# Performance work log

Measured on AMD Instinct MI355X. Metric: run time of the kernel, lower is better.

The kernel has to match this reference:

```python
import jax, jax.numpy as jnp
import numpy as np

B, C, N, T = 16, 32, 1024, 64
C_OUT = 32
ORDER = 2
SMOOTH_DEPTH = 1


def setup_inputs() -> dict:
    key = jax.random.key(0)
    k1, k2, k3, k4 = jax.random.split(key, 4)
    x = jax.random.normal(k1, (B, C, N, T), dtype=jnp.float32)
    # row-normalized dense adjacencies (transition matrices), as used in Graph-WaveNet-style supports
    AL = jax.random.uniform(k2, (N, N), dtype=jnp.float32)
    AL = AL / AL.sum(axis=-1, keepdims=True)
    AS_pos = jax.random.uniform(k3, (N, N), dtype=jnp.float32)
    AS_pos = AS_pos / AS_pos.sum(axis=-1, keepdims=True)
    # 1x1 conv mlp: in_channels = (order*support_len+1)*c_in = 3*C, out_channels = C_OUT
    W_mlp = jax.random.normal(k4, (C_OUT, (ORDER + 1) * C), dtype=jnp.float32) * 0.02
    b_mlp = jnp.zeros((C_OUT,), dtype=jnp.float32)
    return {"x": x, "AL": AL, "AS_pos": AS_pos, "W_mlp": W_mlp, "b_mlp": b_mlp}


def reference(x, AL, AS_pos, W_mlp, b_mlp):
    # gcn_module.forward with short_bool=True, smooth_depth=SMOOTH_DEPTH, eval mode (no dropout)
    ALp = jnp.linalg.matrix_power(AL, SMOOTH_DEPTH)          # [N,N]
    # torch.einsum('bckj,ik->bcij', x, ALp): contract node dim of x against ALp
    x_long = jnp.einsum('ik,bckt->bcit', ALp, x)             # [B,C,N,T]
    x_short = x - x_long
    outs = [x]
    for _ in range(ORDER):
        # dnconv: einsum('nvw,ncwl->ncvl', A, x) with 2D A broadcast over batch
        x_long = jnp.einsum('vw,bcwt->bcvt', AL, x_long)
        x_short = jnp.einsum('vw,bcwt->bcvt', AS_pos, x_short)
        outs.append(x_long + x_short)
    h = jnp.concatenate(outs, axis=1)                        # [B,(ORDER+1)*C,N,T]
    # 1x1 conv == channel mixing
    h = jnp.einsum('oc,bcnt->bont', W_mlp, h) + b_mlp[None, :, None, None]
    return h
```

## Files before the change

kernel.cpp:

```cpp
#include <hip/hip_runtime.h>


typedef __bf16 bf16x8 __attribute__((ext_vector_type(8)));
typedef float f32x4 __attribute__((ext_vector_type(4)));
typedef unsigned int u32x4 __attribute__((ext_vector_type(4)));
typedef unsigned int u32x2 __attribute__((ext_vector_type(2)));

__device__ __forceinline__ unsigned short f2bf(float f) {
  unsigned u = __builtin_bit_cast(unsigned, f);
  u += 0x7fffu + ((u >> 16) & 1u);
  return (unsigned short)(u >> 16);
}
__device__ __forceinline__ float bf2f(unsigned short h) {
  unsigned u = ((unsigned)h) << 16;
  return __builtin_bit_cast(float, u);
}

static constexpr size_t OFF_YC    = 0;
static constexpr size_t OFF_ALBF  = 201326592;
static constexpr size_t OFF_ALT   = OFF_ALBF  + 2097152;
static constexpr size_t OFF_ASBF  = OFF_ALT   + 2097152;
static constexpr size_t OFF_AST   = OFF_ASBF  + 2097152;
static constexpr size_t OFF_AL2   = OFF_AST   + 2097152;
static constexpr size_t OFF_AL2T  = OFF_AL2   + 2097152;
static constexpr size_t OFF_ASAL  = OFF_AL2T  + 2097152;
static constexpr size_t OFF_AS2   = OFF_ASAL  + 2097152;
static constexpr size_t OFF_AL3   = OFF_AS2   + 2097152;
static constexpr size_t OFF_AS2AL = OFF_AL3   + 2097152;
static constexpr size_t OFF_G     = OFF_AS2AL + 2097152;

__global__ __launch_bounds__(256) void k_prep(const float* __restrict__ src,
                                              unsigned short* __restrict__ dstN,
                                              unsigned short* __restrict__ dstT) {
  __shared__ float Xs[64][65];
  const int tid = threadIdx.x;
  const int r0 = blockIdx.x * 64, c0 = blockIdx.y * 64;
  const int lrow = tid >> 4, lc4 = tid & 15;
#pragma unroll
  for (int rr = 0; rr < 4; rr++) {
    int row = rr * 16 + lrow;
    float4 v = *(const float4*)(src + (size_t)(r0 + row) * 1024 + c0 + lc4 * 4);
    Xs[row][lc4 * 4 + 0] = v.x;
    Xs[row][lc4 * 4 + 1] = v.y;
    Xs[row][lc4 * 4 + 2] = v.z;
    Xs[row][lc4 * 4 + 3] = v.w;
    unsigned lo = (unsigned)f2bf(v.x) | ((unsigned)f2bf(v.y) << 16);
    unsigned hi = (unsigned)f2bf(v.z) | ((unsigned)f2bf(v.w) << 16);
    u32x2 pk = {lo, hi};
    *(u32x2*)(dstN + (size_t)(r0 + row) * 1024 + c0 + lc4 * 4) = pk;
  }
  __syncthreads();
  const int wc = tid & 7;
#pragma unroll
  for (int u = 0; u < 2; u++) {
    int t = u * 32 + (tid >> 3);
    unsigned v0 = (unsigned)f2bf(Xs[wc * 8 + 0][t]) | ((unsigned)f2bf(Xs[wc * 8 + 1][t]) << 16);
    unsigned v1 = (unsigned)f2bf(Xs[wc * 8 + 2][t]) | ((unsigned)f2bf(Xs[wc * 8 + 3][t]) << 16);
    unsigned v2 = (unsigned)f2bf(Xs[wc * 8 + 4][t]) | ((unsigned)f2bf(Xs[wc * 8 + 5][t]) << 16);
    unsigned v3 = (unsigned)f2bf(Xs[wc * 8 + 6][t]) | ((unsigned)f2bf(Xs[wc * 8 + 7][t]) << 16);
    u32x4 pk = {v0, v1, v2, v3};
    *(u32x4*)(dstT + (size_t)(c0 + t) * 1024 + r0 + wc * 8) = pk;
  }
}

__device__ __forceinline__ void gemm128_bt(const unsigned short* __restrict__ A,
                                           const unsigned short* __restrict__ Bt,
                                           unsigned short* __restrict__ Cp,
                                           int K, size_t ldc, int m0, int n0) {
  __shared__ unsigned short As[128 * 32];
  __shared__ unsigned short Bs[128 * 32];
  const int tid = threadIdx.x;
  const int wave = tid >> 6, lane = tid & 63;
  const int lane15 = lane & 15, quad = lane >> 4;
  const int wm = wave & 1, wn = wave >> 1;
  const int srow = lane >> 2;
  const int schunk = (lane & 3) * 8;

  const unsigned short* gA0 = A + (size_t)(m0 + wave * 16 + srow) * K + schunk;
  const unsigned short* gA1 = A + (size_t)(m0 + 64 + wave * 16 + srow) * K + schunk;
  const unsigned short* gB0 = Bt + (size_t)(n0 + wave * 16 + srow) * K + schunk;
  const unsigned short* gB1 = Bt + (size_t)(n0 + 64 + wave * 16 + srow) * K + schunk;
  unsigned short* lA0 = As + (wave * 16) * 32;
  unsigned short* lA1 = As + (64 + wave * 16) * 32;
  unsigned short* lB0 = Bs + (wave * 16) * 32;
  unsigned short* lB1 = Bs + (64 + wave * 16) * 32;

  f32x4 acc[4][4];
#pragma unroll
  for (int i = 0; i < 4; i++)
#pragma unroll
    for (int j = 0; j < 4; j++) acc[i][j] = (f32x4){0.f, 0.f, 0.f, 0.f};

  const unsigned short* pa = As + (wm * 64 + lane15) * 32 + quad * 8;
  const unsigned short* pb = Bs + (wn * 64 + lane15) * 32 + quad * 8;

  for (int kb = 0; kb < K; kb += 32) {
    __syncthreads();
    __builtin_amdgcn_global_load_lds(
        (const __attribute__((address_space(1))) unsigned int*)(gA0 + kb),
        (__attribute__((address_space(3))) unsigned int*)lA0, 16, 0, 0);
    __builtin_amdgcn_global_load_lds(
        (const __attribute__((address_space(1))) unsigned int*)(gA1 + kb),
        (__attribute__((address_space(3))) unsigned int*)lA1, 16, 0, 0);
    __builtin_amdgcn_global_load_lds(
        (const __attribute__((address_space(1))) unsigned int*)(gB0 + kb),
        (__attribute__((address_space(3))) unsigned int*)lB0, 16, 0, 0);
    __builtin_amdgcn_global_load_lds(
        (const __attribute__((address_space(1))) unsigned int*)(gB1 + kb),
        (__attribute__((address_space(3))) unsigned int*)lB1, 16, 0, 0);
    __syncthreads();

    bf16x8 av[4], bv[4];
#pragma unroll
    for (int mt = 0; mt < 4; mt++) av[mt] = *(const bf16x8*)(pa + mt * 16 * 32);
#pragma unroll
    for (int nt = 0; nt < 4; nt++) bv[nt] = *(const bf16x8*)(pb + nt * 16 * 32);
#pragma unroll
    for (int mt = 0; mt < 4; mt++)
#pragma unroll
      for (int nt = 0; nt < 4; nt++)
        acc[mt][nt] = __builtin_amdgcn_mfma_f32_16x16x32_bf16(av[mt], bv[nt], acc[mt][nt], 0, 0, 0);
  }

#pragma unroll
  for (int mt = 0; mt < 4; mt++) {
#pragma unroll
    for (int nt = 0; nt < 4; nt++) {
      const int col = n0 + wn * 64 + nt * 16 + lane15;
#pragma unroll
      for (int r = 0; r < 4; r++) {
        const int row = m0 + wm * 64 + mt * 16 + quad * 4 + r;
        Cp[(size_t)row * ldc + col] = f2bf(acc[mt][nt][r]);
      }
    }
  }
}

__global__ __launch_bounds__(256) void k_gemm_pre(char* ws, int stage) {
  const unsigned short* A;
  const unsigned short* Bt;
  unsigned short* Cp;
  const int z = blockIdx.z;
  unsigned short* ALbf = (unsigned short*)(ws + OFF_ALBF);
  unsigned short* ALt  = (unsigned short*)(ws + OFF_ALT);
  unsigned short* ASbf = (unsigned short*)(ws + OFF_ASBF);
  unsigned short* ASt  = (unsigned short*)(ws + OFF_AST);
  unsigned short* AL2  = (unsigned short*)(ws + OFF_AL2);
  unsigned short* ASAL = (unsigned short*)(ws + OFF_ASAL);
  unsigned short* AS2  = (unsigned short*)(ws + OFF_AS2);
  unsigned short* AL3  = (unsigned short*)(ws + OFF_AL3);
  unsigned short* AS2AL= (unsigned short*)(ws + OFF_AS2AL);
  if (stage == 0) {
    if (z == 0)      { A = ALbf; Bt = ALt;  Cp = AL2;  }
    else if (z == 1) { A = ASbf; Bt = ALt;  Cp = ASAL; }
    else             { A = ASbf; Bt = ASt;  Cp = AS2;  }
  } else {
    if (z == 0)      { A = AL2;  Bt = ALt;  Cp = AL3;  }
    else             { A = AS2;  Bt = ALt;  Cp = AS2AL;}
  }
  gemm128_bt(A, Bt, Cp, 1024, 1024, blockIdx.y * 128, blockIdx.x * 128);
}

__global__ __launch_bounds__(256) void k_assemble_G(const unsigned short* __restrict__ AL2,
                                                    const unsigned short* __restrict__ ASAL,
                                                    const float* __restrict__ ASf,
                                                    const unsigned short* __restrict__ AL3,
                                                    const unsigned short* __restrict__ AS2,
                                                    const unsigned short* __restrict__ AS2AL,
                                                    const float* __restrict__ W,
                                                    unsigned short* __restrict__ Wall,
                                                    unsigned short* __restrict__ G) {
  if (blockIdx.x == 0) {
    for (int k = threadIdx.x; k < 3072; k += 256) {
      int oo = k >> 5, c = k & 31;
      Wall[k] = f2bf(W[(oo & 31) * 96 + (oo >> 5) * 32 + c]);
    }
  }
  int i = blockIdx.x * 256 + threadIdx.x;
  int r = i >> 10, c = i & 1023;
  float g1 = bf2f(AL2[i]) + ASf[i] - bf2f(ASAL[i]);
  float g2 = bf2f(AL3[i]) + bf2f(AS2[i]) - bf2f(AS2AL[i]);
  G[(size_t)r * 2048 + c]        = f2bf(g1);
  G[(size_t)r * 2048 + 1024 + c] = f2bf(g2);
}

__global__ __launch_bounds__(256, 8) void k_mix_g(const float* __restrict__ x,
                                                  const unsigned short* __restrict__ Wall,
                                                  unsigned short* __restrict__ Yc) {
  const int tid = threadIdx.x;
  const int sid = (blockIdx.x & 7) * 256 + (blockIdx.x >> 3);
  const int b   = sid >> 7;
  const int n8g = sid & 127;
  const int nbase = n8g * 8;
  const int wave = tid >> 6, lane = tid & 63;
  const int lane15 = lane & 15, quad = lane >> 4;
  const int t = wave * 16 + lane15;

  bf16x8 afr[6];
#pragma unroll
  for (int ot = 0; ot < 6; ot++)
    afr[ot] = *(const bf16x8*)(Wall + (ot * 16 + lane15) * 32 + quad * 8);

  const float* xb = x + (size_t)b * 2097152 + (size_t)(quad * 8) * 65536 + t;

  bf16x8 bfr[8];
#pragma unroll
  for (int nl = 0; nl < 8; nl++) {
    const float* xp = xb + (size_t)(nbase + nl) * 64;
    unsigned u[4];
#pragma unroll
    for (int e = 0; e < 4; e++) {
      float a  = xp[(size_t)(2 * e) * 65536];
      float c2 = xp[(size_t)(2 * e + 1) * 65536];
      u[e] = (unsigned)f2bf(a) | ((unsigned)f2bf(c2) << 16);
    }
    u32x4 pk = {u[0], u[1], u[2], u[3]};
    bfr[nl] = __builtin_bit_cast(bf16x8, pk);
  }

#pragma unroll
  for (int ot = 0; ot < 6; ot++) {
    f32x4 acc[8];
    const f32x4 z = (f32x4){0.f, 0.f, 0.f, 0.f};
#pragma unroll
    for (int nl = 0; nl < 8; nl++)
      acc[nl] = __builtin_amdgcn_mfma_f32_16x16x32_bf16(afr[ot], bfr[nl], z, 0, 0, 0);
    const int og = ot >> 1;
    const int o  = (ot & 1) * 16 + quad * 4;
    const size_t plane = (size_t)(og * 128 + n8g) * 262144;
#pragma unroll
    for (int r = 0; r < 4; r++) {
      unsigned u0 = (unsigned)f2bf(acc[0][r]) | ((unsigned)f2bf(acc[1][r]) << 16);
      unsigned u1 = (unsigned)f2bf(acc[2][r]) | ((unsigned)f2bf(acc[3][r]) << 16);
      unsigned u2 = (unsigned)f2bf(acc[4][r]) | ((unsigned)f2bf(acc[5][r]) << 16);
      unsigned u3 = (unsigned)f2bf(acc[6][r]) | ((unsigned)f2bf(acc[7][r]) << 16);
      u32x4 pk = {u0, u1, u2, u3};
      size_t j = (size_t)(b * 32 + o + r) * 64 + t;
      *(u32x4*)(Yc + plane + j * 8) = pk;
    }
  }
}

__global__ __launch_bounds__(512) void k_gemm_main8(const unsigned short* __restrict__ A,
                                                    const unsigned short* __restrict__ Yc,
                                                    const float* __restrict__ bm,
                                                    float* __restrict__ out) {
  __shared__ unsigned short lds[65536];
  const int tid = threadIdx.x;
  const int wave = tid >> 6, lane = tid & 63;
  const int lane15 = lane & 15, quad = lane >> 4;
  const int wr = wave >> 2, wc = wave & 3;

  const int bid = blockIdx.x;
  const int swz = (bid & 7) * 64 + (bid >> 3);
  const int nx = swz >> 2, my = swz & 3;
  const int m0 = my * 256, n0 = nx * 256;

  const int srow = tid >> 3;
  const int cB   = (tid & 7) ^ (srow & 7);
  const int skc  = cB << 3;
  const int ldst0 = (tid & ~63) << 3;

#define STAGE_A(rowbase, ldsptr, ktile)                                                 \
  do {                                                                                  \
    const unsigned short* _g =                                                          \
        A + (size_t)((rowbase) + srow) * 2048 + (size_t)((ktile) * 64 + skc);           \
    __builtin_amdgcn_global_load_lds(                                                   \
        (const __attribute__((address_space(1))) unsigned int*)_g,                      \
        (__attribute__((address_space(3))) unsigned int*)((ldsptr) + ldst0), 16, 0, 0); \
    __builtin_amdgcn_global_load_lds(                                                   \
        (const __attribute__((address_space(1))) unsigned int*)(_g + 131072),           \
        (__attribute__((address_space(3))) unsigned int*)((ldsptr) + 4096 + ldst0),     \
        16, 0, 0);                                                                      \
  } while (0)

#define STAGE_B(rowbase, ldsptr, ktile)                                                 \
  do {                                                                                  \
    const unsigned short* _g = Yc + (size_t)(128 + (ktile) * 8 + cB) * 262144 +         \
                               (size_t)((rowbase) + srow) * 8;                          \
    __builtin_amdgcn_global_load_lds(                                                   \
        (const __attribute__((address_space(1))) unsigned int*)_g,                      \
        (__attribute__((address_space(3))) unsigned int*)((ldsptr) + ldst0), 16, 0, 0); \
    __builtin_amdgcn_global_load_lds(                                                   \
        (const __attribute__((address_space(1))) unsigned int*)(_g + 512),              \
        (__attribute__((address_space(3))) unsigned int*)((ldsptr) + 4096 + ldst0),     \
        16, 0, 0);                                                                      \
  } while (0)

#define RD_BFR()                                                                        \
  _Pragma("unroll") for (int n = 0; n < 4; n++)                                         \
      _Pragma("unroll") for (int kk = 0; kk < 2; kk++)                                  \
          bfr[n][kk] = *(const bf16x8*)(pB + n * 1024 + aks[kk]);

#define RD_AFR(FR, mA, mB)                                                              \
  _Pragma("unroll") for (int kk = 0; kk < 2; kk++) {                                    \
    FR[0][kk] = *(const bf16x8*)(pA + (mA) * 1024 + aks[kk]);                           \
    FR[1][kk] = *(const bf16x8*)(pA + (mB) * 1024 + aks[kk]);                           \
  }

#define MFMA2(i0, FR)                                                                   \
  _Pragma("unroll") for (int kk = 0; kk < 2; kk++)                                      \
      _Pragma("unroll") for (int mi = 0; mi < 2; mi++)                                  \
          _Pragma("unroll") for (int n = 0; n < 4; n++)                                 \
              acc[(i0) + mi][n] = __builtin_amdgcn_mfma_f32_16x16x32_bf16(              \
                  FR[mi][kk], bfr[n][kk], acc[(i0) + mi][n], 0, 0, 0);

#define SAFEBAR()                                                                       \
  asm volatile("s_waitcnt lgkmcnt(0)" ::: "memory");                                    \
  __builtin_amdgcn_s_barrier();
#define LGKM0() asm volatile("s_waitcnt lgkmcnt(0)" ::: "memory");                      \
                __builtin_amdgcn_sched_barrier(0);
#define PRIO1() __builtin_amdgcn_s_setprio(1);
#define PRIO0() __builtin_amdgcn_s_setprio(0);

  unsigned short* Acur = lds;
  unsigned short* Bcur = lds + 16384;
  unsigned short* Aalt = lds + 32768;
  unsigned short* Balt = lds + 49152;

  f32x4 acc[8][4];
#pragma unroll
  for (int i = 0; i < 8; i++)
#pragma unroll
    for (int j = 0; j < 4; j++) acc[i][j] = (f32x4){0.f, 0.f, 0.f, 0.f};

  const int swz8 = (lane15 & 7) << 3;
  int aks[2];
  aks[0] = (quad << 3) ^ swz8;
  aks[1] = (32 | (quad << 3)) ^ swz8;

  bf16x8 bfr[4][2], afrP[2][2], afrQ[2][2];

  STAGE_B(n0,       Bcur,        0);
  STAGE_B(n0 + 128, Bcur + 8192, 0);
  STAGE_A(m0,       Acur,        0);
  STAGE_A(m0 + 128, Acur + 8192, 0);
  STAGE_B(n0,       Balt,        1);
  STAGE_B(n0 + 128, Balt + 8192, 1);
  STAGE_A(m0,       Aalt,        1);
  asm volatile("s_waitcnt vmcnt(6)" ::: "memory");

  for (int u = 0; u < 30; ++u) {
    const unsigned short* pA = Acur + (wr * 128 + lane15) * 64;
    const unsigned short* pB = Bcur + (wc * 64 + lane15) * 64;
    SAFEBAR();
    RD_BFR();
    RD_AFR(afrP, 0, 1);
    LGKM0();
    PRIO1(); MFMA2(0, afrP); PRIO0();
    RD_AFR(afrQ, 2, 3);
    STAGE_A(m0 + 128, Aalt + 8192, u + 1);
    SAFEBAR();
    __builtin_amdgcn_sched_barrier(0);
    PRIO1(); MFMA2(2, afrQ); PRIO0();
    RD_AFR(afrP, 4, 5);
    STAGE_B(n0, Bcur, u + 2);
    SAFEBAR();
    __builtin_amdgcn_sched_barrier(0);
    PRIO1(); MFMA2(4, afrP); PRIO0();
    RD_AFR(afrQ, 6, 7);
    STAGE_B(n0 + 128, Bcur + 8192, u + 2);
    SAFEBAR();
    __builtin_amdgcn_sched_barrier(0);
    PRIO1(); MFMA2(6, afrQ); PRIO0();
    STAGE_A(m0, Acur, u + 2);
    asm volatile("s_waitcnt vmcnt(4)" ::: "memory");
    unsigned short* t;
    t = Acur; Acur = Aalt; Aalt = t;
    t = Bcur; Bcur = Balt; Balt = t;
  }

  {
    const unsigned short* pA = Acur + (wr * 128 + lane15) * 64;
    const unsigned short* pB = Bcur + (wc * 64 + lane15) * 64;
    SAFEBAR();
    RD_BFR();
    RD_AFR(afrP, 0, 1);
    LGKM0();
    PRIO1(); MFMA2(0, afrP); PRIO0();
    RD_AFR(afrQ, 2, 3);
    STAGE_A(m0 + 128, Aalt + 8192, 31);
    SAFEBAR();
    __builtin_amdgcn_sched_barrier(0);
    PRIO1(); MFMA2(2, afrQ); PRIO0();
    RD_AFR(afrP, 4, 5);
    SAFEBAR();
    __builtin_amdgcn_sched_barrier(0);
    PRIO1(); MFMA2(4, afrP); PRIO0();
    RD_AFR(afrQ, 6, 7);
    SAFEBAR();
    __builtin_amdgcn_sched_barrier(0);
    PRIO1(); MFMA2(6, afrQ); PRIO0();
    asm volatile("s_waitcnt vmcnt(0)" ::: "memory");
    SAFEBAR();
    unsigned short* t;
    t = Acur; Acur = Aalt; Aalt = t;
    t = Bcur; Bcur = Balt; Balt = t;
  }

  {
    const unsigned short* pA = Acur + (wr * 128 + lane15) * 64;
    const unsigned short* pB = Bcur + (wc * 64 + lane15) * 64;
    RD_BFR();
#pragma unroll
    for (int p = 0; p < 4; p++) {
      bf16x8 afr[2][2];
#pragma unroll
      for (int mi = 0; mi < 2; mi++)
#pragma unroll
        for (int kk = 0; kk < 2; kk++)
          afr[mi][kk] = *(const bf16x8*)(pA + (2 * p + mi) * 1024 + aks[kk]);
#pragma unroll
      for (int kk = 0; kk < 2; kk++)
#pragma unroll
        for (int mi = 0; mi < 2; mi++)
#pragma unroll
          for (int n = 0; n < 4; n++)
            acc[2 * p + mi][n] = __builtin_amdgcn_mfma_f32_16x16x32_bf16(
                afr[mi][kk], bfr[n][kk], acc[2 * p + mi][n], 0, 0, 0);
    }
  }

#pragma unroll
  for (int mt = 0; mt < 8; mt++) {
    const int row = m0 + wr * 128 + mt * 16 + quad * 4;
#pragma unroll
    for (int nf = 0; nf < 4; nf++) {
      const int col = n0 + wc * 64 + nf * 16 + lane15;
      const int bo_idx = col >> 6;
      const float bo = bm[bo_idx & 31];
      const size_t obase = (size_t)bo_idx * 65536 + (col & 63);
      ushort4 yv = *(const ushort4*)(Yc + (size_t)(row >> 3) * 262144 +
                                     (size_t)col * 8 + (row & 7));
      out[obase + (size_t)(row + 0) * 64] = acc[mt][nf][0] + bf2f(yv.x) + bo;
      out[obase + (size_t)(row + 1) * 64] = acc[mt][nf][1] + bf2f(yv.y) + bo;
      out[obase + (size_t)(row + 2) * 64] = acc[mt][nf][2] + bf2f(yv.z) + bo;
      out[obase + (size_t)(row + 3) * 64] = acc[mt][nf][3] + bf2f(yv.w) + bo;
    }
  }
#undef STAGE_A
#undef STAGE_B
#undef RD_BFR
#undef RD_AFR
#undef MFMA2
#undef SAFEBAR
#undef LGKM0
#undef PRIO1
#undef PRIO0
}

extern "C" void kernel_launch(void* const* d_in, const int* in_sizes, int n_in,
                              void* d_out, int out_size, void* d_ws, size_t ws_size,
                              hipStream_t stream) {
  const float* x  = (const float*)d_in[0];
  const float* AL = (const float*)d_in[1];
  const float* AS = (const float*)d_in[2];
  const float* W  = (const float*)d_in[3];
  const float* bm = (const float*)d_in[4];
  float* out = (float*)d_out;
  char* ws = (char*)d_ws;

  unsigned short* Yc    = (unsigned short*)(ws + OFF_YC);
  unsigned short* ALbf  = (unsigned short*)(ws + OFF_ALBF);
  unsigned short* ALt   = (unsigned short*)(ws + OFF_ALT);
  unsigned short* ASbf  = (unsigned short*)(ws + OFF_ASBF);
  unsigned short* ASt   = (unsigned short*)(ws + OFF_AST);
  unsigned short* AL2   = (unsigned short*)(ws + OFF_AL2);
  unsigned short* ASAL  = (unsigned short*)(ws + OFF_ASAL);
  unsigned short* AS2   = (unsigned short*)(ws + OFF_AS2);
  unsigned short* AL3   = (unsigned short*)(ws + OFF_AL3);
  unsigned short* AS2AL = (unsigned short*)(ws + OFF_AS2AL);
  unsigned short* Gm    = (unsigned short*)(ws + OFF_G);
  unsigned short* Wall  = (unsigned short*)(ws + OFF_ALBF);

  k_prep<<<dim3(16, 16, 1), 256, 0, stream>>>(AL, ALbf, ALt);
  k_prep<<<dim3(16, 16, 1), 256, 0, stream>>>(AS, ASbf, ASt);
  k_gemm_pre<<<dim3(8, 8, 3), 256, 0, stream>>>(ws, 0);
  k_gemm_pre<<<dim3(8, 8, 2), 256, 0, stream>>>(ws, 1);
  k_assemble_G<<<4096, 256, 0, stream>>>(AL2, ASAL, AS, AL3, AS2, AS2AL, W, Wall, Gm);
  k_mix_g<<<2048, 256, 0, stream>>>(x, Wall, Yc);
  k_gemm_main8<<<dim3(512, 1, 1), 512, 0, stream>>>(Gm, Yc, bm, out);
}
```

Baseline: 518.0 us.

## Reschedule main GEMM pipeline barriers and merge two prep launches

The main bf16 MFMA GEMM loop gets a new schedule. Barriers now bracket each MFMA group with explicit lgkmcnt waits, a single A fragment register set replaces the two, and A-tile staging is reordered so Aalt loads are issued inside the loop instead of before it. The last full iteration is written as its own block that matches the new schedule. Separately, the two k_prep launches for AL and AS become one launch that picks its matrix from blockIdx.z, removing one kernel launch. The added barriers could increase synchronisation stalls, and the new ordering of LDS buffer reuse risks read/write hazards.

```diff
diff --git a/kernel.cpp b/kernel.cpp
--- a/kernel.cpp
+++ b/kernel.cpp
@@ -29,9 +29,15 @@
 static constexpr size_t OFF_AS2AL = OFF_AL3   + 2097152;
 static constexpr size_t OFF_G     = OFF_AS2AL + 2097152;
 
-__global__ __launch_bounds__(256) void k_prep(const float* __restrict__ src,
-                                              unsigned short* __restrict__ dstN,
-                                              unsigned short* __restrict__ dstT) {
+__global__ __launch_bounds__(256) void k_prep(const float* __restrict__ AL,
+                                              const float* __restrict__ AS,
+                                              unsigned short* __restrict__ ALn,
+                                              unsigned short* __restrict__ ALtr,
+                                              unsigned short* __restrict__ ASn,
+                                              unsigned short* __restrict__ AStr) {
+  const float* src = blockIdx.z ? AS : AL;
+  unsigned short* dstN = blockIdx.z ? ASn : ALn;
+  unsigned short* dstT = blockIdx.z ? AStr : ALtr;
   __shared__ float Xs[64][65];
   const int tid = threadIdx.x;
   const int r0 = blockIdx.x * 64, c0 = blockIdx.y * 64;
@@ -292,24 +298,23 @@
       _Pragma("unroll") for (int kk = 0; kk < 2; kk++)                                  \
           bfr[n][kk] = *(const bf16x8*)(pB + n * 1024 + aks[kk]);
 
-#define RD_AFR(FR, mA, mB)                                                              \
+#define RD_AFR(mA, mB)                                                                  \
   _Pragma("unroll") for (int kk = 0; kk < 2; kk++) {                                    \
-    FR[0][kk] = *(const bf16x8*)(pA + (mA) * 1024 + aks[kk]);                           \
-    FR[1][kk] = *(const bf16x8*)(pA + (mB) * 1024 + aks[kk]);                           \
-  }
-
-#define MFMA2(i0, FR)                                                                   \
+    afr[0][kk] = *(const bf16x8*)(pA + (mA) * 1024 + aks[kk]);                          \
+    afr[1][kk] = *(const bf16x8*)(pA + (mB) * 1024 + aks[kk]);                          \
+  }
+
+#define MFMA2(i0)                                                                       \
   _Pragma("unroll") for (int kk = 0; kk < 2; kk++)                                      \
       _Pragma("unroll") for (int mi = 0; mi < 2; mi++)                                  \
           _Pragma("unroll") for (int n = 0; n < 4; n++)                                 \
               acc[(i0) + mi][n] = __builtin_amdgcn_mfma_f32_16x16x32_bf16(              \
-                  FR[mi][kk], bfr[n][kk], acc[(i0) + mi][n], 0, 0, 0);
-
-#define SAFEBAR()                                                                       \
-  asm volatile("s_waitcnt lgkmcnt(0)" ::: "memory");                                    \
-  __builtin_amdgcn_s_barrier();
+                  afr[mi][kk], bfr[n][kk], acc[(i0) + mi][n], 0, 0, 0);
+
+#define BAR()   asm volatile("" ::: "memory"); __builtin_amdgcn_s_barrier();
 #define LGKM0() asm volatile("s_waitcnt lgkmcnt(0)" ::: "memory");                      \
                 __builtin_amdgcn_sched_barrier(0);
+#define LGKM8() asm volatile("s_waitcnt lgkmcnt(8)" ::: "memory");
 #define PRIO1() __builtin_amdgcn_s_setprio(1);
 #define PRIO0() __builtin_amdgcn_s_setprio(0);
 
@@ -329,95 +334,86 @@
   aks[0] = (quad << 3) ^ swz8;
   aks[1] = (32 | (quad << 3)) ^ swz8;
 
-  bf16x8 bfr[4][2], afrP[2][2], afrQ[2][2];
-
+  bf16x8 bfr[4][2], afr[2][2];
+
+  STAGE_A(m0,       Acur,        0);
+  STAGE_A(m0 + 128, Acur + 8192, 0);
   STAGE_B(n0,       Bcur,        0);
   STAGE_B(n0 + 128, Bcur + 8192, 0);
-  STAGE_A(m0,       Acur,        0);
-  STAGE_A(m0 + 128, Acur + 8192, 0);
   STAGE_B(n0,       Balt,        1);
   STAGE_B(n0 + 128, Balt + 8192, 1);
-  STAGE_A(m0,       Aalt,        1);
-  asm volatile("s_waitcnt vmcnt(6)" ::: "memory");
-
-  for (int u = 0; u < 30; ++u) {
+  asm volatile("s_waitcnt vmcnt(4)" ::: "memory");
+  BAR();
+
+  for (int t = 0; t < 30; ++t) {
     const unsigned short* pA = Acur + (wr * 128 + lane15) * 64;
     const unsigned short* pB = Bcur + (wc * 64 + lane15) * 64;
-    SAFEBAR();
     RD_BFR();
-    RD_AFR(afrP, 0, 1);
-    LGKM0();
-    PRIO1(); MFMA2(0, afrP); PRIO0();
-    RD_AFR(afrQ, 2, 3);
-    STAGE_A(m0 + 128, Aalt + 8192, u + 1);
-    SAFEBAR();
-    __builtin_amdgcn_sched_barrier(0);
-    PRIO1(); MFMA2(2, afrQ); PRIO0();
-    RD_AFR(afrP, 4, 5);
-    STAGE_B(n0, Bcur, u + 2);
-    SAFEBAR();
-    __builtin_amdgcn_sched_barrier(0);
-    PRIO1(); MFMA2(4, afrP); PRIO0();
-    RD_AFR(afrQ, 6, 7);
-    STAGE_B(n0 + 128, Bcur + 8192, u + 2);
-    SAFEBAR();
-    __builtin_amdgcn_sched_barrier(0);
-    PRIO1(); MFMA2(6, afrQ); PRIO0();
-    STAGE_A(m0, Acur, u + 2);
+    RD_AFR(0, 1);
+    STAGE_A(m0, Aalt, t + 1);
+    LGKM8();
+    BAR(); LGKM0();
+    PRIO1(); MFMA2(0); PRIO0();
+    BAR();
+    RD_AFR(2, 3);
+    STAGE_A(m0 + 128, Aalt + 8192, t + 1);
+    BAR(); LGKM0();
+    PRIO1(); MFMA2(2); PRIO0();
+    BAR();
+    RD_AFR(4, 5);
+    STAGE_B(n0, Bcur, t + 2);
+    BAR(); LGKM0();
+    PRIO1(); MFMA2(4); PRIO0();
+    BAR();
+    RD_AFR(6, 7);
+    STAGE_B(n0 + 128, Bcur + 8192, t + 2);
+    BAR(); LGKM0();
+    PRIO1(); MFMA2(6); PRIO0();
     asm volatile("s_waitcnt vmcnt(4)" ::: "memory");
-    unsigned short* t;
-    t = Acur; Acur = Aalt; Aalt = t;
-    t = Bcur; Bcur = Balt; Balt = t;
-  }
-
-  {
-    const unsigned short* pA = Acur + (wr * 128 + lane15) * 64;
-    const unsigned short* pB = Bcur + (wc * 64 + lane15) * 64;
-    SAFEBAR();
-    RD_BFR();
-    RD_AFR(afrP, 0, 1);
-    LGKM0();
-    PRIO1(); MFMA2(0, afrP); PRIO0();
-    RD_AFR(afrQ, 2, 3);
-    STAGE_A(m0 + 128, Aalt + 8192, 31);
-    SAFEBAR();
-    __builtin_amdgcn_sched_barrier(0);
-    PRIO1(); MFMA2(2, afrQ); PRIO0();
-    RD_AFR(afrP, 4, 5);
-    SAFEBAR();
-    __builtin_amdgcn_sched_barrier(0);
-    PRIO1(); MFMA2(4, afrP); PRIO0();
-    RD_AFR(afrQ, 6, 7);
-    SAFEBAR();
-    __builtin_amdgcn_sched_barrier(0);
-    PRIO1(); MFMA2(6, afrQ); PRIO0();
-    asm volatile("s_waitcnt vmcnt(0)" ::: "memory");
-    SAFEBAR();
-    unsigned short* t;
-    t = Acur; Acur = Aalt; Aalt = t;
-    t = Bcur; Bcur = Balt; Balt = t;
+    BAR();
+    unsigned short* tmp;
+    tmp = Acur; Acur = Aalt; Aalt = tmp;
+    tmp = Bcur; Bcur = Balt; Balt = tmp;
   }
 
   {
     const unsigned short* pA = Acur + (wr * 128 + lane15) * 64;
     const unsigned short* pB = Bcur + (wc * 64 + lane15) * 64;
     RD_BFR();
+    RD_AFR(0, 1);
+    STAGE_A(m0, Aalt, 31);
+    LGKM8();
+    BAR(); LGKM0();
+    PRIO1(); MFMA2(0); PRIO0();
+    BAR();
+    RD_AFR(2, 3);
+    STAGE_A(m0 + 128, Aalt + 8192, 31);
+    BAR(); LGKM0();
+    PRIO1(); MFMA2(2); PRIO0();
+    BAR();
+    RD_AFR(4, 5);
+    BAR(); LGKM0();
+    PRIO1(); MFMA2(4); PRIO0();
+    BAR();
+    RD_AFR(6, 7);
+    BAR(); LGKM0();
+    PRIO1(); MFMA2(6); PRIO0();
+    asm volatile("s_waitcnt vmcnt(0)" ::: "memory");
+    BAR();
+    unsigned short* tmp;
+    tmp = Acur; Acur = Aalt; Aalt = tmp;
+    tmp = Bcur; Bcur = Balt; Balt = tmp;
+  }
+
+  {
+    const unsigned short* pA = Acur + (wr * 128 + lane15) * 64;
+    const unsigned short* pB = Bcur + (wc * 64 + lane15) * 64;
+    RD_BFR();
 #pragma unroll
     for (int p = 0; p < 4; p++) {
-      bf16x8 afr[2][2];
-#pragma unroll
-      for (int mi = 0; mi < 2; mi++)
-#pragma unroll
-        for (int kk = 0; kk < 2; kk++)
-          afr[mi][kk] = *(const bf16x8*)(pA + (2 * p + mi) * 1024 + aks[kk]);
-#pragma unroll
-      for (int kk = 0; kk < 2; kk++)
-#pragma unroll
-        for (int mi = 0; mi < 2; mi++)
-#pragma unroll
-          for (int n = 0; n < 4; n++)
-            acc[2 * p + mi][n] = __builtin_amdgcn_mfma_f32_16x16x32_bf16(
-                afr[mi][kk], bfr[n][kk], acc[2 * p + mi][n], 0, 0, 0);
+      RD_AFR(2 * p, 2 * p + 1);
+      LGKM0();
+      MFMA2(2 * p);
     }
   }
 
@@ -443,8 +439,9 @@
 #undef RD_BFR
 #undef RD_AFR
 #undef MFMA2
-#undef SAFEBAR
+#undef BAR
 #undef LGKM0
+#undef LGKM8
 #undef PRIO1
 #undef PRIO0
 }
@@ -473,8 +470,7 @@
   unsigned short* Gm    = (unsigned short*)(ws + OFF_G);
   unsigned short* Wall  = (unsigned short*)(ws + OFF_ALBF);
 
-  k_prep<<<dim3(16, 16, 1), 256, 0, stream>>>(AL, ALbf, ALt);
-  k_prep<<<dim3(16, 16, 1), 256, 0, stream>>>(AS, ASbf, ASt);
+  k_prep<<<dim3(16, 16, 2), 256, 0, stream>>>(AL, AS, ALbf, ALt, ASbf, ASt);
   k_gemm_pre<<<dim3(8, 8, 3), 256, 0, stream>>>(ws, 0);
   k_gemm_pre<<<dim3(8, 8, 2), 256, 0, stream>>>(ws, 1);
   k_assemble_G<<<4096, 256, 0, stream>>>(AL2, ASAL, AS, AL3, AS2, AS2AL, W, Wall, Gm);
```

Measured after the change: 511.2 us. Within noise of the previous version (-1.3%).
